# Performance work log

Measured on AMD Instinct MI355X. Metric: run time of the kernel, lower is better.

Reference implementation:

```python
import jax, jax.numpy as jnp
import numpy as np


def setup_inputs() -> dict:
    key = jax.random.key(0)
    ks = jax.random.split(key, 10)
    B, S, C, H, NC, T = 128, 512, 512, 512, 64, 25
    s = 0.02  # init scale
    return {
        "x": jax.random.normal(ks[0], (B, S, C), jnp.float32),
        "text": jax.random.randint(ks[1], (B, T + 1), 0, NC),
        "W_i2h": jax.random.normal(ks[2], (C, H), jnp.float32) * s,
        "W_h2h": jax.random.normal(ks[3], (H, H), jnp.float32) * s,
        "b_h2h": jnp.zeros((H,), jnp.float32),
        "W_score": jax.random.normal(ks[4], (H, 1), jnp.float32) * s,
        "W_lstm": jax.random.normal(ks[5], (C + NC, 4 * H), jnp.float32) * s,
        "U_lstm": jax.random.normal(ks[6], (H, 4 * H), jnp.float32) * s,
        "b_lstm": jnp.zeros((4 * H,), jnp.float32),
        "W_gen": jax.random.normal(ks[7], (H, NC), jnp.float32) * s,
        "b_gen": jnp.zeros((NC,), jnp.float32),
        "batch_max_length": 25,
    }


def reference(x, text, W_i2h, W_h2h, b_h2h, W_score, W_lstm, U_lstm, b_lstm,
              W_gen, b_gen, batch_max_length):
    B = x.shape[0]
    H = W_h2h.shape[0]
    NC = W_gen.shape[1]
    T = batch_max_length

    # i2h(batch_H) is loop-invariant -> compute once. [B,S,H]
    batch_H_proj = jnp.einsum('bsc,ch->bsh', x, W_i2h)
    # one-hot teacher-forcing inputs, time-major for scan. [T,B,NC]
    onehots_t = jnp.swapaxes(jax.nn.one_hot(text[:, :T], NC, dtype=x.dtype), 0, 1)

    def step(carry, char_oh):
        h, c = carry
        hp = (h @ W_h2h + b_h2h)[:, None, :]                 # [B,1,H]
        e = jnp.tanh(batch_H_proj + hp) @ W_score            # [B,S,1]
        alpha = jax.nn.softmax(e, axis=1)                    # [B,S,1]
        context = jnp.einsum('bs,bsc->bc', alpha[..., 0], x) # [B,C]
        inp = jnp.concatenate([context, char_oh], axis=1)    # [B,C+NC]
        # Keras LSTMCell gate math: z split into i,f,g,o chunks
        z = inp @ W_lstm + h @ U_lstm + b_lstm               # [B,4H]
        zi, zf, zg, zo = jnp.split(z, 4, axis=1)
        i = jax.nn.sigmoid(zi)
        f = jax.nn.sigmoid(zf)
        g = jnp.tanh(zg)
        o = jax.nn.sigmoid(zo)
        c_new = f * c + i * g
        h_new = o * jnp.tanh(c_new)
        return (h_new, c_new), h_new

    init = (jnp.zeros((B, H), x.dtype), jnp.zeros((B, H), x.dtype))
    _, hs = jax.lax.scan(step, init, onehots_t)              # [T,B,H]
    output_hiddens = jnp.swapaxes(hs, 0, 1)                  # [B,T,H]
    probs = output_hiddens @ W_gen + b_gen                   # [B,T,NC]
    return probs
```

## Files before the change

### kernel.cpp

```cpp
#include <hip/hip_runtime.h>
#include <hip/hip_bf16.h>

#define B_ 128
#define S_ 512
#define C_ 512
#define H_ 512
#define NC_ 64
#define T_ 25
#define TEXTW (T_ + 1)

typedef __attribute__((ext_vector_type(8))) short bf16x8;
typedef __attribute__((ext_vector_type(8))) unsigned short u16x8;
typedef __attribute__((ext_vector_type(4))) float f32x4;

__device__ __forceinline__ float bf2f(unsigned short u) {
    union { unsigned int i; float f; } v; v.i = ((unsigned int)u) << 16; return v.f;
}
__device__ __forceinline__ unsigned short f2bf(float f) {
    union { float f; unsigned int u; } v; v.f = f;
    unsigned int r = (v.u + 0x7FFFu + ((v.u >> 16) & 1u)) >> 16;
    return (unsigned short)r;
}
__device__ __forceinline__ void gload_lds16(const void* g, void* l) {
    __builtin_amdgcn_global_load_lds(
        (const __attribute__((address_space(1))) unsigned int*)g,
        (__attribute__((address_space(3))) unsigned int*)l, 16, 0, 0);
}
__device__ __forceinline__ float fast_tanh(float x) {
    float e = __builtin_amdgcn_exp2f(2.885390082f * x);
    return 1.f - 2.f * __builtin_amdgcn_rcpf(e + 1.f);
}
__device__ __forceinline__ float fast_sigmoid(float x) {
    return __builtin_amdgcn_rcpf(1.f + __builtin_amdgcn_exp2f(-1.442695041f * x));
}

__global__ __launch_bounds__(512) void setup_k(
    const float* __restrict__ Wi, const float* __restrict__ Wh,
    const float* __restrict__ Wl, const float* __restrict__ Ul,
    unsigned short* __restrict__ Wt_bf, unsigned short* __restrict__ Wh_bf,
    unsigned short* __restrict__ WU_t,
    float* __restrict__ c2, unsigned short* __restrict__ inp) {
    int blk = blockIdx.x, tid = threadIdx.x;
    if (blk < 128) {
        c2[blk * 512 + tid] = 0.f;
        c2[65536 + blk * 512 + tid] = 0.f;
        inp[blk * 1024 + 512 + tid] = 0;
    } else if (blk < 640) {
        int n = blk - 128;
        Wt_bf[n * 512 + tid] = f2bf(Wi[tid * 512 + n]);
    } else if (blk < 1152) {
        int i = (blk - 640) * 512 + tid;
        Wh_bf[i] = f2bf(Wh[i]);
    } else {
        int np = blk - 1152;
        int h = np >> 2, g = np & 3;
        {
            float v = Wl[(size_t)tid * 2048 + g * 512 + h];
            WU_t[(size_t)np * 1024 + tid] = f2bf(v);
        }
        {
            float v = Ul[(size_t)tid * 2048 + g * 512 + h];
            WU_t[(size_t)np * 1024 + 512 + tid] = f2bf(v);
        }
    }
}

__global__ __launch_bounds__(256) void conv_x(const float* __restrict__ in,
                                              unsigned short* __restrict__ out) {
    int i = blockIdx.x * 256 + threadIdx.x;
    const float4 v = ((const float4*)in)[i];
    ushort4 o;
    o.x = f2bf(v.x); o.y = f2bf(v.y); o.z = f2bf(v.z); o.w = f2bf(v.w);
    ((ushort4*)out)[i] = o;
}

__global__ __launch_bounds__(256) void gemm_proj(const unsigned short* __restrict__ A,
                                                 const unsigned short* __restrict__ Bt,
                                                 unsigned short* __restrict__ Cm) {
    __shared__ unsigned short As[128 * 64];
    __shared__ unsigned short Bs[128 * 64];
    int tid = threadIdx.x;
    int lane = tid & 63;
    int wid = tid >> 6;
    int wr = wid >> 1, wc = wid & 1;
    int row0 = blockIdx.y * 128;
    int col0 = blockIdx.x * 128;

    f32x4 acc[4][4];
#pragma unroll
    for (int i = 0; i < 4; ++i)
#pragma unroll
        for (int j = 0; j < 4; ++j) acc[i][j] = (f32x4){0.f, 0.f, 0.f, 0.f};

    for (int k0 = 0; k0 < 512; k0 += 64) {
#pragma unroll
        for (int i = 0; i < 4; ++i) {
            int e = tid + i * 256;
            int r = e >> 3, cc = e & 7;
            int cs = cc ^ (r & 7);
            gload_lds16(A + (size_t)(row0 + r) * 512 + k0 + cs * 8, &As[e * 8]);
        }
#pragma unroll
        for (int i = 0; i < 4; ++i) {
            int e = tid + i * 256;
            int r = e >> 3, cc = e & 7;
            int cs = cc ^ (r & 7);
            gload_lds16(Bt + (size_t)(col0 + r) * 512 + k0 + cs * 8, &Bs[e * 8]);
        }
        __syncthreads();
#pragma unroll
        for (int ks = 0; ks < 2; ++ks) {
            bf16x8 a[4], b[4];
#pragma unroll
            for (int i = 0; i < 4; ++i) {
                int m = wr * 64 + i * 16 + (lane & 15);
                int ch = (ks * 4 + (lane >> 4)) ^ (m & 7);
                a[i] = *(const bf16x8*)&As[(m * 8 + ch) * 8];
            }
#pragma unroll
            for (int j = 0; j < 4; ++j) {
                int n = wc * 64 + j * 16 + (lane & 15);
                int ch = (ks * 4 + (lane >> 4)) ^ (n & 7);
                b[j] = *(const bf16x8*)&Bs[(n * 8 + ch) * 8];
            }
#pragma unroll
            for (int i = 0; i < 4; ++i)
#pragma unroll
                for (int j = 0; j < 4; ++j)
                    acc[i][j] = __builtin_amdgcn_mfma_f32_16x16x32_bf16(a[i], b[j], acc[i][j], 0, 0, 0);
        }
        __syncthreads();
    }
#pragma unroll
    for (int i = 0; i < 4; ++i)
#pragma unroll
        for (int j = 0; j < 4; ++j) {
            int gcol = col0 + wc * 64 + j * 16 + (lane & 15);
#pragma unroll
            for (int r = 0; r < 4; ++r) {
                int grow = row0 + wr * 64 + i * 16 + (lane >> 4) * 4 + r;
                Cm[(size_t)grow * 512 + gcol] = f2bf(acc[i][j][r]);
            }
        }
}

__global__ __launch_bounds__(512) void z_gemm(
    const unsigned short* __restrict__ inp, const unsigned short* __restrict__ Bt,
    const float* __restrict__ pc, const float* __restrict__ pm,
    const float* __restrict__ ps, float* __restrict__ Z) {
    __shared__ unsigned short As[128 * 128];
    __shared__ unsigned short Bs[64 * 128];
    int tid = threadIdx.x;
    int lane = tid & 63;
    int wave = tid >> 6;
    int wr = wave >> 2, wc = wave & 3;
    int col0 = blockIdx.x * 64;

    float cw0[4], cw1[4];
    int rr[4], csv[4];
#pragma unroll
    for (int i = 0; i < 4; ++i) {
        int e = tid + i * 512;
        int r = e >> 4, cc = e & 15;
        rr[i] = r; csv[i] = cc ^ (r & 15);
        float m0 = pm[r], m1 = pm[128 + r];
        float s0 = ps[r], s1 = ps[128 + r];
        float M = fmaxf(m0, m1);
        float w0 = __builtin_amdgcn_exp2f(1.442695041f * (m0 - M));
        float w1 = __builtin_amdgcn_exp2f(1.442695041f * (m1 - M));
        float inv = 1.f / (w0 * s0 + w1 * s1);
        cw0[i] = w0 * inv; cw1[i] = w1 * inv;
    }

    f32x4 acc[4];
#pragma unroll
    for (int i = 0; i < 4; ++i) acc[i] = (f32x4){0.f, 0.f, 0.f, 0.f};

    for (int k0 = 0; k0 < 1024; k0 += 128) {
        if (k0 < 512) {
#pragma unroll
            for (int i = 0; i < 4; ++i) {
                int e = tid + i * 512;
                int kb = k0 + csv[i] * 8;
                const float* c0p = pc + rr[i] * 512 + kb;
                const float* c1p = pc + 65536 + rr[i] * 512 + kb;
                float4 c0a = *(const float4*)c0p;
                float4 c0b = *(const float4*)(c0p + 4);
                float4 c1a = *(const float4*)c1p;
                float4 c1b = *(const float4*)(c1p + 4);
                u16x8 o;
                o[0] = f2bf(cw0[i] * c0a.x + cw1[i] * c1a.x);
                o[1] = f2bf(cw0[i] * c0a.y + cw1[i] * c1a.y);
                o[2] = f2bf(cw0[i] * c0a.z + cw1[i] * c1a.z);
                o[3] = f2bf(cw0[i] * c0a.w + cw1[i] * c1a.w);
                o[4] = f2bf(cw0[i] * c0b.x + cw1[i] * c1b.x);
                o[5] = f2bf(cw0[i] * c0b.y + cw1[i] * c1b.y);
                o[6] = f2bf(cw0[i] * c0b.z + cw1[i] * c1b.z);
                o[7] = f2bf(cw0[i] * c0b.w + cw1[i] * c1b.w);
                *(u16x8*)&As[e * 8] = o;
            }
        } else {
#pragma unroll
            for (int i = 0; i < 4; ++i) {
                int e = tid + i * 512;
                gload_lds16(inp + (size_t)rr[i] * 1024 + k0 + csv[i] * 8, &As[e * 8]);
            }
        }
#pragma unroll
        for (int i = 0; i < 2; ++i) {
            int e = tid + i * 512;
            int r = e >> 4, cc = e & 15;
            int cs = cc ^ (r & 15);
            gload_lds16(Bt + (size_t)(col0 + r) * 1024 + k0 + cs * 8, &Bs[e * 8]);
        }
        __syncthreads();
#pragma unroll
        for (int ks = 0; ks < 4; ++ks) {
            bf16x8 a[4], bfr;
#pragma unroll
            for (int i = 0; i < 4; ++i) {
                int m = wr * 64 + i * 16 + (lane & 15);
                int ch = (ks * 4 + (lane >> 4)) ^ (m & 15);
                a[i] = *(const bf16x8*)&As[(m * 16 + ch) * 8];
            }
            {
                int n = wc * 16 + (lane & 15);
                int ch = (ks * 4 + (lane >> 4)) ^ (n & 15);
                bfr = *(const bf16x8*)&Bs[(n * 16 + ch) * 8];
            }
#pragma unroll
            for (int i = 0; i < 4; ++i)
                acc[i] = __builtin_amdgcn_mfma_f32_16x16x32_bf16(a[i], bfr, acc[i], 0, 0, 0);
        }
        __syncthreads();
    }
#pragma unroll
    for (int i = 0; i < 4; ++i) {
        int gcol = col0 + wc * 16 + (lane & 15);
#pragma unroll
        for (int r = 0; r < 4; ++r) {
            int grow = wr * 64 + i * 16 + (lane >> 4) * 4 + r;
            Z[(size_t)grow * 2048 + gcol] = acc[i][r];
        }
    }
}

__global__ __launch_bounds__(1024) void ghp_e2(
    const float* __restrict__ z, const int* __restrict__ text,
    const float* __restrict__ Wl, const float* __restrict__ bl,
    const unsigned short* __restrict__ Whb, const float* __restrict__ bh2h,
    float* __restrict__ c2, float* __restrict__ hs_t,
    unsigned short* __restrict__ inp,
    const unsigned short* __restrict__ proj, const unsigned short* __restrict__ xb,
    const float* __restrict__ Wscore,
    float* __restrict__ pc, float* __restrict__ pm, float* __restrict__ ps, int t) {
    __shared__ float shg[512];
    __shared__ float gp[16][512];
    __shared__ float sh_hp[512];
    __shared__ float sh_e[256];
    __shared__ float sh_alpha[256];
    __shared__ float sh_red[8];
    __shared__ float shp[8][512];
    int blk = blockIdx.x;
    int half = blk >> 7, b = blk & 127;
    int tid = threadIdx.x, wave = tid >> 6, lane = tid & 63;

    if (t >= 0) {
        if (tid < 512) {
            int ch = text[b * TEXTW + t];
            const float* wrow = Wl + (size_t)(512 + ch) * 2048;
            float4 zv = *(const float4*)(z + (size_t)b * 2048 + tid * 4);
            float zi = zv.x + bl[tid] + wrow[tid];
            float zf = zv.y + bl[512 + tid] + wrow[512 + tid];
            float zg = zv.z + bl[1024 + tid] + wrow[1024 + tid];
            float zo = zv.w + bl[1536 + tid] + wrow[1536 + tid];
            float ig = fast_sigmoid(zi);
            float fg = fast_sigmoid(zf);
            float gg = fast_tanh(zg);
            float og = fast_sigmoid(zo);
            int idx = half * 65536 + b * 512 + tid;
            float cn = fg * c2[idx] + ig * gg;
            c2[idx] = cn;
            float hn = og * fast_tanh(cn);
            if (half == 0) {
                hs_t[b * 512 + tid] = hn;
                inp[b * 1024 + 512 + tid] = f2bf(hn);
            }
            shg[tid] = hn;
        }
        __syncthreads();
        if (t >= T_ - 1) return;
        {
            float r8[8] = {0.f, 0.f, 0.f, 0.f, 0.f, 0.f, 0.f, 0.f};
#pragma unroll 4
            for (int kk = 0; kk < 32; ++kk) {
                int k = wave * 32 + kk;
                float hv = shg[k];
                u16x8 wv = *(const u16x8*)(Whb + k * 512 + lane * 8);
#pragma unroll
                for (int jj = 0; jj < 8; ++jj) r8[jj] = fmaf(hv, bf2f(wv[jj]), r8[jj]);
            }
#pragma unroll
            for (int jj = 0; jj < 8; ++jj) gp[wave][lane * 8 + jj] = r8[jj];
        }
        __syncthreads();
        if (tid < 512) {
            float s = bh2h[tid];
#pragma unroll
            for (int w = 0; w < 16; ++w) s += gp[w][tid];
            sh_hp[tid] = s;
        }
        __syncthreads();
    } else {
        if (tid < 512) sh_hp[tid] = bh2h[tid];
        __syncthreads();
    }

    {
        float4 h0 = *(const float4*)(sh_hp + lane * 8);
        float4 h1 = *(const float4*)(sh_hp + lane * 8 + 4);
        float4 w0 = *(const float4*)(Wscore + lane * 8);
        float4 w1 = *(const float4*)(Wscore + lane * 8 + 4);
        float hp_r[8] = {h0.x, h0.y, h0.z, h0.w, h1.x, h1.y, h1.z, h1.w};
        float w_r[8]  = {w0.x, w0.y, w0.z, w0.w, w1.x, w1.y, w1.z, w1.w};
        float w2_r[8];
#pragma unroll
        for (int j = 0; j < 8; ++j) w2_r[j] = -2.f * w_r[j];
        int s0g = half * 256 + wave * 16;
        for (int i = 0; i < 16; i += 4) {
            bf16x8 pv[4];
#pragma unroll
            for (int q = 0; q < 4; ++q)
                pv[q] = *(const bf16x8*)(proj + ((size_t)(b * 512 + s0g + i + q) << 9) + lane * 8);
#pragma unroll
            for (int q = 0; q < 4; ++q) {
                float a = 0.f;
#pragma unroll
                for (int j = 0; j < 8; ++j) {
                    float xv = bf2f((unsigned short)pv[q][j]) + hp_r[j];
                    float r = __builtin_amdgcn_rcpf(__builtin_amdgcn_exp2f(2.885390082f * xv) + 1.f);
                    a += w_r[j];
                    a = fmaf(w2_r[j], r, a);
                }
#pragma unroll
                for (int off = 32; off > 0; off >>= 1) a += __shfl_xor(a, off, 64);
                if (lane == 0) sh_e[wave * 16 + i + q] = a;
            }
        }
    }
    __syncthreads();

    if (tid < 256) {
        float v = sh_e[tid];
        float m = v;
#pragma unroll
        for (int off = 32; off > 0; off >>= 1) m = fmaxf(m, __shfl_xor(m, off, 64));
        if (lane == 0) sh_red[wave] = m;
    }
    __syncthreads();
    if (tid < 256) {
        float mh = fmaxf(fmaxf(sh_red[0], sh_red[1]), fmaxf(sh_red[2], sh_red[3]));
        float p = __builtin_amdgcn_exp2f(1.442695041f * (sh_e[tid] - mh));
        float ss = p;
#pragma unroll
        for (int off = 32; off > 0; off >>= 1) ss += __shfl_xor(ss, off, 64);
        if (lane == 0) sh_red[4 + wave] = ss;
        sh_alpha[tid] = p;
    }
    __syncthreads();
    if (tid == 0) {
        pm[half * 128 + b] = fmaxf(fmaxf(sh_red[0], sh_red[1]), fmaxf(sh_red[2], sh_red[3]));
        ps[half * 128 + b] = sh_red[4] + sh_red[5] + sh_red[6] + sh_red[7];
    }

    {
        int cc = wave >> 3, sg = wave & 7;
        int col = cc * 256 + lane * 4;
        float a0 = 0.f, a1 = 0.f, a2 = 0.f, a3 = 0.f;
#pragma unroll 4
        for (int sl = sg; sl < 256; sl += 8) {
            float al = sh_alpha[sl];
            int s = half * 256 + sl;
            ushort4 xv = *(const ushort4*)(xb + ((size_t)(b * 512 + s) << 9) + col);
            a0 = fmaf(al, bf2f(xv.x), a0);
            a1 = fmaf(al, bf2f(xv.y), a1);
            a2 = fmaf(al, bf2f(xv.z), a2);
            a3 = fmaf(al, bf2f(xv.w), a3);
        }
        *(float4*)&shp[sg][col] = make_float4(a0, a1, a2, a3);
    }
    __syncthreads();
    if (tid < 512) {
        float s = 0.f;
#pragma unroll
        for (int r = 0; r < 8; ++r) s += shp[r][tid];
        pc[(size_t)(half * 128 + b) * 512 + tid] = s;
    }
}

__global__ __launch_bounds__(64) void gen_probs(const float* __restrict__ hs,
                                                const float* __restrict__ Wg,
                                                const float* __restrict__ bg,
                                                float* __restrict__ out) {
    __shared__ float sh[512];
    int bt = blockIdx.x;
    int b = bt / T_, t = bt % T_;
    int tid = threadIdx.x;
    const float* hrow = hs + ((size_t)t * B_ + b) * H_;
    for (int i = tid; i < 512; i += 64) sh[i] = hrow[i];
    __syncthreads();
    float acc = bg[tid];
#pragma unroll 4
    for (int k = 0; k < 512; ++k) acc = fmaf(sh[k], Wg[k * 64 + tid], acc);
    out[(size_t)bt * 64 + tid] = acc;
}

extern "C" void kernel_launch(void* const* d_in, const int* in_sizes, int n_in,
                              void* d_out, int out_size, void* d_ws, size_t ws_size,
                              hipStream_t stream) {
    const float* x       = (const float*)d_in[0];
    const int*   text    = (const int*)d_in[1];
    const float* W_i2h   = (const float*)d_in[2];
    const float* W_h2h   = (const float*)d_in[3];
    const float* b_h2h   = (const float*)d_in[4];
    const float* W_score = (const float*)d_in[5];
    const float* W_lstm  = (const float*)d_in[6];
    const float* U_lstm  = (const float*)d_in[7];
    const float* b_lstm  = (const float*)d_in[8];
    const float* W_gen   = (const float*)d_in[9];
    const float* b_gen   = (const float*)d_in[10];
    float* out = (float*)d_out;

    char* ws = (char*)d_ws;
    unsigned short* x_bf    = (unsigned short*)ws;
    unsigned short* proj_bf = (unsigned short*)(ws + 67108864);
    unsigned short* Wt_bf   = (unsigned short*)(ws + 134217728);
    unsigned short* Wh_bf   = (unsigned short*)(ws + 134742016);
    unsigned short* WU_t    = (unsigned short*)(ws + 135266304);
    float* c2      = (float*)(ws + 139460608);
    unsigned short* inp_bf = (unsigned short*)(ws + 139984896);
    float* z_buf   = (float*)(ws + 140247040);
    float* pc      = (float*)(ws + 141295616);
    float* pm      = (float*)(ws + 141819904);
    float* ps      = (float*)(ws + 141820928);
    float* hs      = (float*)(ws + 141821952);

    setup_k<<<dim3(3200), 512, 0, stream>>>(W_i2h, W_h2h, W_lstm, U_lstm,
                                            Wt_bf, Wh_bf, WU_t, c2, inp_bf);
    conv_x<<<dim3(32768), 256, 0, stream>>>(x, x_bf);
    gemm_proj<<<dim3(4, 512), 256, 0, stream>>>(x_bf, Wt_bf, proj_bf);
    ghp_e2<<<dim3(256), 1024, 0, stream>>>(z_buf, text, W_lstm, b_lstm, Wh_bf, b_h2h,
                                           c2, hs, inp_bf, proj_bf, x_bf, W_score,
                                           pc, pm, ps, -1);
    for (int t = 0; t < T_; ++t) {
        z_gemm<<<dim3(32), 512, 0, stream>>>(inp_bf, WU_t, pc, pm, ps, z_buf);
        ghp_e2<<<dim3(256), 1024, 0, stream>>>(z_buf, text, W_lstm, b_lstm, Wh_bf, b_h2h,
                                               c2, hs + (size_t)t * (B_ * H_),
                                               inp_bf, proj_bf, x_bf, W_score,
                                               pc, pm, ps, t);
    }
    gen_probs<<<dim3(B_ * T_), 64, 0, stream>>>(hs, W_gen, b_gen, out);
}
```

Before: 1.401 ms.

## Fuse attention scores, softmax and context via online softmax; batch gen_probs rows

```diff
diff --git a/kernel.cpp b/kernel.cpp
--- a/kernel.cpp
+++ b/kernel.cpp
@@ -255,12 +255,9 @@
     const float* __restrict__ Wscore,
     float* __restrict__ pc, float* __restrict__ pm, float* __restrict__ ps, int t) {
     __shared__ float shg[512];
-    __shared__ float gp[16][512];
+    __shared__ float wk[16][512];
     __shared__ float sh_hp[512];
-    __shared__ float sh_e[256];
-    __shared__ float sh_alpha[256];
-    __shared__ float sh_red[8];
-    __shared__ float shp[8][512];
+    __shared__ float sh_red[32];
     int blk = blockIdx.x;
     int half = blk >> 7, b = blk & 127;
     int tid = threadIdx.x, wave = tid >> 6, lane = tid & 63;
@@ -301,13 +298,13 @@
                 for (int jj = 0; jj < 8; ++jj) r8[jj] = fmaf(hv, bf2f(wv[jj]), r8[jj]);
             }
 #pragma unroll
-            for (int jj = 0; jj < 8; ++jj) gp[wave][lane * 8 + jj] = r8[jj];
+            for (int jj = 0; jj < 8; ++jj) wk[wave][lane * 8 + jj] = r8[jj];
         }
         __syncthreads();
         if (tid < 512) {
             float s = bh2h[tid];
 #pragma unroll
-            for (int w = 0; w < 16; ++w) s += gp[w][tid];
+            for (int w = 0; w < 16; ++w) s += wk[w][tid];
             sh_hp[tid] = s;
         }
         __syncthreads();
@@ -326,75 +323,56 @@
         float w2_r[8];
 #pragma unroll
         for (int j = 0; j < 8; ++j) w2_r[j] = -2.f * w_r[j];
+        int j0 = lane * 8;
+        float m_run = -1e30f, s_run = 0.f;
+        float ctx[8] = {0.f, 0.f, 0.f, 0.f, 0.f, 0.f, 0.f, 0.f};
         int s0g = half * 256 + wave * 16;
-        for (int i = 0; i < 16; i += 4) {
-            bf16x8 pv[4];
-#pragma unroll
-            for (int q = 0; q < 4; ++q)
-                pv[q] = *(const bf16x8*)(proj + ((size_t)(b * 512 + s0g + i + q) << 9) + lane * 8);
-#pragma unroll
-            for (int q = 0; q < 4; ++q) {
-                float a = 0.f;
-#pragma unroll
-                for (int j = 0; j < 8; ++j) {
-                    float xv = bf2f((unsigned short)pv[q][j]) + hp_r[j];
-                    float r = __builtin_amdgcn_rcpf(__builtin_amdgcn_exp2f(2.885390082f * xv) + 1.f);
-                    a += w_r[j];
-                    a = fmaf(w2_r[j], r, a);
-                }
-#pragma unroll
-                for (int off = 32; off > 0; off >>= 1) a += __shfl_xor(a, off, 64);
-                if (lane == 0) sh_e[wave * 16 + i + q] = a;
-            }
-        }
+#pragma unroll 2
+        for (int i = 0; i < 16; ++i) {
+            size_t rowoff = ((size_t)(b * 512 + s0g + i) << 9);
+            const bf16x8 pv = *(const bf16x8*)(proj + rowoff + j0);
+            const u16x8 xv = *(const u16x8*)(xb + rowoff + j0);
+            float a = 0.f;
+#pragma unroll
+            for (int j = 0; j < 8; ++j) {
+                float xvv = bf2f((unsigned short)pv[j]) + hp_r[j];
+                float r = __builtin_amdgcn_rcpf(__builtin_amdgcn_exp2f(2.885390082f * xvv) + 1.f);
+                a += w_r[j];
+                a = fmaf(w2_r[j], r, a);
+            }
+#pragma unroll
+            for (int off = 32; off > 0; off >>= 1) a += __shfl_xor(a, off, 64);
+            if (a > m_run) {
+                float sc = __builtin_amdgcn_exp2f(1.442695041f * (m_run - a));
+                s_run *= sc;
+#pragma unroll
+                for (int j = 0; j < 8; ++j) ctx[j] *= sc;
+                m_run = a;
+            }
+            float p = __builtin_amdgcn_exp2f(1.442695041f * (a - m_run));
+            s_run += p;
+#pragma unroll
+            for (int j = 0; j < 8; ++j) ctx[j] = fmaf(p, bf2f(xv[j]), ctx[j]);
+        }
+        if (lane == 0) { sh_red[wave] = m_run; sh_red[16 + wave] = s_run; }
+#pragma unroll
+        for (int j = 0; j < 8; ++j) wk[wave][j0 + j] = ctx[j];
     }
     __syncthreads();
 
-    if (tid < 256) {
-        float v = sh_e[tid];
-        float m = v;
-#pragma unroll
-        for (int off = 32; off > 0; off >>= 1) m = fmaxf(m, __shfl_xor(m, off, 64));
-        if (lane == 0) sh_red[wave] = m;
-    }
-    __syncthreads();
-    if (tid < 256) {
-        float mh = fmaxf(fmaxf(sh_red[0], sh_red[1]), fmaxf(sh_red[2], sh_red[3]));
-        float p = __builtin_amdgcn_exp2f(1.442695041f * (sh_e[tid] - mh));
-        float ss = p;
-#pragma unroll
-        for (int off = 32; off > 0; off >>= 1) ss += __shfl_xor(ss, off, 64);
-        if (lane == 0) sh_red[4 + wave] = ss;
-        sh_alpha[tid] = p;
-    }
-    __syncthreads();
-    if (tid == 0) {
-        pm[half * 128 + b] = fmaxf(fmaxf(sh_red[0], sh_red[1]), fmaxf(sh_red[2], sh_red[3]));
-        ps[half * 128 + b] = sh_red[4] + sh_red[5] + sh_red[6] + sh_red[7];
-    }
-
-    {
-        int cc = wave >> 3, sg = wave & 7;
-        int col = cc * 256 + lane * 4;
-        float a0 = 0.f, a1 = 0.f, a2 = 0.f, a3 = 0.f;
-#pragma unroll 4
-        for (int sl = sg; sl < 256; sl += 8) {
-            float al = sh_alpha[sl];
-            int s = half * 256 + sl;
-            ushort4 xv = *(const ushort4*)(xb + ((size_t)(b * 512 + s) << 9) + col);
-            a0 = fmaf(al, bf2f(xv.x), a0);
-            a1 = fmaf(al, bf2f(xv.y), a1);
-            a2 = fmaf(al, bf2f(xv.z), a2);
-            a3 = fmaf(al, bf2f(xv.w), a3);
-        }
-        *(float4*)&shp[sg][col] = make_float4(a0, a1, a2, a3);
-    }
-    __syncthreads();
     if (tid < 512) {
-        float s = 0.f;
-#pragma unroll
-        for (int r = 0; r < 8; ++r) s += shp[r][tid];
-        pc[(size_t)(half * 128 + b) * 512 + tid] = s;
+        float M = sh_red[0];
+#pragma unroll
+        for (int w = 1; w < 16; ++w) M = fmaxf(M, sh_red[w]);
+        float ssum = 0.f, csum = 0.f;
+#pragma unroll
+        for (int w = 0; w < 16; ++w) {
+            float sc = __builtin_amdgcn_exp2f(1.442695041f * (sh_red[w] - M));
+            ssum = fmaf(sc, sh_red[16 + w], ssum);
+            csum = fmaf(sc, wk[w][tid], csum);
+        }
+        pc[(size_t)(half * 128 + b) * 512 + tid] = csum;
+        if (tid == 0) { pm[half * 128 + b] = M; ps[half * 128 + b] = ssum; }
     }
 }
 
@@ -402,17 +380,28 @@
                                                 const float* __restrict__ Wg,
                                                 const float* __restrict__ bg,
                                                 float* __restrict__ out) {
-    __shared__ float sh[512];
-    int bt = blockIdx.x;
-    int b = bt / T_, t = bt % T_;
+    __shared__ float sh[8][512];
+    int r0 = blockIdx.x * 8;
     int tid = threadIdx.x;
-    const float* hrow = hs + ((size_t)t * B_ + b) * H_;
-    for (int i = tid; i < 512; i += 64) sh[i] = hrow[i];
+#pragma unroll
+    for (int q = 0; q < 8; ++q) {
+        int row = r0 + q;
+        int b = row / T_, t = row % T_;
+        const float* hrow = hs + ((size_t)t * B_ + b) * H_;
+        for (int i = tid; i < 512; i += 64) sh[q][i] = hrow[i];
+    }
     __syncthreads();
-    float acc = bg[tid];
+    float acc[8];
+#pragma unroll
+    for (int q = 0; q < 8; ++q) acc[q] = bg[tid];
 #pragma unroll 4
-    for (int k = 0; k < 512; ++k) acc = fmaf(sh[k], Wg[k * 64 + tid], acc);
-    out[(size_t)bt * 64 + tid] = acc;
+    for (int k = 0; k < 512; ++k) {
+        float w = Wg[k * 64 + tid];
+#pragma unroll
+        for (int q = 0; q < 8; ++q) acc[q] = fmaf(sh[q][k], w, acc[q]);
+    }
+#pragma unroll
+    for (int q = 0; q < 8; ++q) out[(size_t)(r0 + q) * 64 + tid] = acc[q];
 }
 
 extern "C" void kernel_launch(void* const* d_in, const int* in_sizes, int n_in,
@@ -459,5 +448,5 @@
                                                inp_bf, proj_bf, x_bf, W_score,
                                                pc, pm, ps, t);
     }
-    gen_probs<<<dim3(B_ * T_), 64, 0, stream>>>(hs, W_gen, b_gen, out);
-}
+    gen_probs<<<dim3(400), 64, 0, stream>>>(hs, W_gen, b_gen, out);
+}
```

New measurement: 1.476 ms. 5.3% more time.
